# Performance work log

Hardware: AMD Instinct MI355X
Metric: run time of the kernel (lower is better)

The kernel has to match this reference:

```python
import jax, jax.numpy as jnp
import numpy as np

EPS = 1e-5
GROUPS = 4


def gconv1x1(x, w, b, groups):
    # x: [B,C,H,W]; w: [Cout, Cin//groups]; grouped 1x1 conv
    B, C, H, W = x.shape
    Co = w.shape[0]
    xg = x.reshape(B, groups, C // groups, H, W)
    wg = w.reshape(groups, Co // groups, C // groups)
    y = jnp.einsum('bgchw,goc->bgohw', xg, wg).reshape(B, Co, H, W)
    if b is not None:
        y = y + b[None, :, None, None]
    return y


def setup_inputs() -> dict:
    key = jax.random.key(0)
    ks = jax.random.split(key, 9)
    B, C, H, W = 8, 64, 160, 160
    Cq = C // 8
    s = 0.1
    return {
        'x': jax.random.normal(ks[0], (B, C, H, W), jnp.float32),
        'wq': jax.random.normal(ks[1], (Cq, C // GROUPS), jnp.float32) * s,
        'bq': jax.random.normal(ks[2], (Cq,), jnp.float32) * s,
        'wk': jax.random.normal(ks[3], (Cq, C // GROUPS), jnp.float32) * s,
        'bk': jax.random.normal(ks[4], (Cq,), jnp.float32) * s,
        'wv': jax.random.normal(ks[5], (C, C // GROUPS), jnp.float32) * s,
        'bv': jax.random.normal(ks[6], (C,), jnp.float32) * s,
        'gamma': jax.random.normal(ks[7], (1,), jnp.float32) * s,
        'w1d': jax.random.normal(ks[8], (C, C // GROUPS), jnp.float32) * s,
        'bn_w': jnp.ones((C,), jnp.float32),
        'bn_b': jnp.zeros((C,), jnp.float32),
    }


def reference(x, wq, bq, wk, bk, wv, bv, gamma, w1d, bn_w, bn_b):
    B, C, H, W = x.shape
    q = gconv1x1(x, wq, bq, GROUPS)   # [B,Cq,H,W]
    k = gconv1x1(x, wk, bk, GROUPS)   # [B,Cq,H,W]
    v = gconv1x1(x, wv, bv, GROUPS)   # [B,C,H,W]

    # column (H) attention energies with -inf diagonal (self excluded on H path)
    energy_H = jnp.einsum('bchw,bcjw->bhwj', q, k)  # [B,H,W,H]
    diag = jnp.where(jnp.eye(H, dtype=bool), -jnp.inf, 0.0).astype(x.dtype)
    energy_H = energy_H + diag[:, None, :]
    # row (W) attention energies
    energy_W = jnp.einsum('bchw,bchj->bhwj', q, k)  # [B,H,W,W]

    att = jax.nn.softmax(jnp.concatenate([energy_H, energy_W], axis=3), axis=3)
    att_H = att[..., :H]           # [B,H,W,H]
    att_W = att[..., H:]           # [B,H,W,W]

    out_H = jnp.einsum('bcjw,bhwj->bchw', v, att_H)
    out_W = jnp.einsum('bchj,bhwj->bchw', v, att_W)
    out = gamma[0] * (out_H + out_W)               # [B,C,H,W]

    # kernel-size-1 grouped conv1d (dilation irrelevant for k=1), no bias
    L = H * W
    o = out.reshape(B, GROUPS, C // GROUPS, L)
    w1g = w1d.reshape(GROUPS, C // GROUPS, C // GROUPS)
    o = jnp.einsum('bgcl,goc->bgol', o, w1g).reshape(B, C, L)

    # BatchNorm1d (training mode: batch stats over (B, L), biased variance)
    mean = jnp.mean(o, axis=(0, 2), keepdims=True)
    var = jnp.mean((o - mean) ** 2, axis=(0, 2), keepdims=True)
    o = (o - mean) / jnp.sqrt(var + EPS) * bn_w[None, :, None] + bn_b[None, :, None]

    o = o.reshape(B, C, H, W)
    return jax.nn.relu(o + x)
```

## Files before the change

### kernel.cpp

```cpp
#include <hip/hip_runtime.h>
#include <math.h>

#define B_ 8
#define C_ 64
#define H_ 160
#define W_ 160
#define HW_ (H_*W_)

typedef _Float16 h2 __attribute__((ext_vector_type(2)));
typedef _Float16 h8 __attribute__((ext_vector_type(8)));
typedef float f4v __attribute__((ext_vector_type(4)));
union H8u { h8 v; h2 h[4]; };

__device__ inline float fdot2(h2 a, h2 b, float c) {
    return __builtin_amdgcn_fdot2(a, b, c, false);
}
__device__ inline float dot16(const float4* xr, const float* wr, float acc) {
    float4 a = xr[0], b = xr[1], c = xr[2], d = xr[3];
    acc += a.x*wr[0]  + a.y*wr[1]  + a.z*wr[2]  + a.w*wr[3];
    acc += b.x*wr[4]  + b.y*wr[5]  + b.z*wr[6]  + b.w*wr[7];
    acc += c.x*wr[8]  + c.y*wr[9]  + c.z*wr[10] + c.w*wr[11];
    acc += d.x*wr[12] + d.y*wr[13] + d.z*wr[14] + d.w*wr[15];
    return acc;
}

static constexpr size_t N_PIX  = (size_t)B_*H_*W_;
static constexpr size_t N_FULL = (size_t)B_*H_*W_*C_;
static constexpr size_t OFF_OUTH  = 0;
static constexpr size_t OFF_VROW  = N_FULL/2;
static constexpr size_t OFF_QROW  = OFF_VROW + N_FULL/2;
static constexpr size_t OFF_KROW  = OFF_QROW + N_PIX*4;
static constexpr size_t OFF_MH    = OFF_KROW + N_PIX*4;
static constexpr size_t OFF_SH    = OFF_MH + N_PIX;
static constexpr size_t OFF_BNSUM = OFF_SH + N_PIX;
static constexpr size_t OFF_BNSQ  = OFF_BNSUM + 64;

__global__ __launch_bounds__(256,4) void qkv_kernel(
    const float* __restrict__ x,
    const float* __restrict__ wq, const float* __restrict__ bq,
    const float* __restrict__ wk, const float* __restrict__ bk,
    const float* __restrict__ wv, const float* __restrict__ bv,
    _Float16* __restrict__ qrow, _Float16* __restrict__ krow,
    _Float16* __restrict__ vrow)
{
    __shared__ __align__(16) float xs[128][68];
    const int tid = threadIdx.x;
    const int w0 = blockIdx.x * 32;
    const int h0 = blockIdx.y * 4;
    const int b  = blockIdx.z;

    const float* xb = x + (size_t)b*C_*HW_;
    for (int i = tid; i < 2048; i += 256) {
        int w4 = i & 7;
        int c  = ((i >> 3) & 7) | (((i >> 6) & 7) << 3);
        int hh = i >> 9;
        float4 v = *(const float4*)(xb + (size_t)c*HW_ + (size_t)(h0+hh)*W_ + w0 + w4*4);
        int pix = hh*32 + w4*4;
        xs[pix+0][c] = v.x; xs[pix+1][c] = v.y; xs[pix+2][c] = v.z; xs[pix+3][c] = v.w;
    }
    __syncthreads();

    float resv[32];
    {
        const int cp = tid & 31, pg = tid >> 5;
        const int c0 = 2*cp, g = c0 >> 4;
        float w0r[16], w1r[16];
        #pragma unroll
        for (int p = 0; p < 4; p++) {
            *(float4*)&w0r[4*p] = ((const float4*)(wv + c0*16))[p];
            *(float4*)&w1r[4*p] = ((const float4*)(wv + (c0+1)*16))[p];
        }
        const float b0 = bv[c0], b1 = bv[c0+1];
        #pragma unroll 4
        for (int i = 0; i < 16; i++) {
            int pix = pg*16 + i;
            const float4* xr = (const float4*)&xs[pix][g*16];
            resv[2*i]   = dot16(xr, w0r, b0);
            resv[2*i+1] = dot16(xr, w1r, b1);
        }
    }
    float resqk[8];
    {
        const int out = tid & 15, pg = tid >> 4;
        const int cq = out & 7, g = cq >> 1;
        const float* wp = ((out < 8) ? wq : wk) + cq*16;
        const float bb = (out < 8) ? bq[cq] : bk[cq];
        float wr[16];
        #pragma unroll
        for (int p = 0; p < 4; p++) *(float4*)&wr[4*p] = ((const float4*)wp)[p];
        #pragma unroll
        for (int i = 0; i < 8; i++) {
            int pix = pg*8 + i;
            resqk[i] = dot16((const float4*)&xs[pix][g*16], wr, bb);
        }
    }
    __syncthreads();

    unsigned* vs32 = (unsigned*)&xs[0][0];
    unsigned* qk32 = vs32 + 4096;
    {
        const int cp = tid & 31, pg = tid >> 5;
        #pragma unroll
        for (int i = 0; i < 16; i++) {
            int pix = pg*16 + i;
            h2 p; p.x = (_Float16)resv[2*i]; p.y = (_Float16)resv[2*i+1];
            vs32[pix*32 + cp] = *(unsigned*)&p;
        }
    }
    {
        const int out = tid & 15, pg = tid >> 4;
        _Float16* qks = (_Float16*)qk32;
        #pragma unroll
        for (int i = 0; i < 8; i++) qks[(pg*8+i)*16 + out] = (_Float16)resqk[i];
    }
    __syncthreads();

    unsigned* vrow32 = (unsigned*)vrow;
    for (int i = tid; i < 4096; i += 256) {
        int pix = i >> 5, cp = i & 31;
        size_t bp = ((size_t)b*H_ + h0 + (pix>>5))*W_ + w0 + (pix & 31);
        vrow32[bp*32 + cp] = vs32[i];
    }
    unsigned* qrow32 = (unsigned*)qrow;
    unsigned* krow32 = (unsigned*)krow;
    for (int i = tid; i < 1024; i += 256) {
        int pix = i >> 3, part = i & 7;
        size_t bp = ((size_t)b*H_ + h0 + (pix>>5))*W_ + w0 + (pix & 31);
        unsigned val = qk32[pix*8 + part];
        if (part < 4) qrow32[bp*4 + part]     = val;
        else          krow32[bp*4 + part - 4] = val;
    }
}

__global__ __launch_bounds__(256,4) void passA_kernel(
    const _Float16* __restrict__ qrow, const _Float16* __restrict__ krow,
    const _Float16* __restrict__ vrow,
    _Float16* __restrict__ outH, float* __restrict__ mH, float* __restrict__ sH)
{
    __shared__ __align__(16) _Float16 pool[10240];
    __shared__ __align__(16) _Float16 q2h[160][8];
    __shared__ __align__(16) _Float16 k2h[160][8];

    _Float16* v2s = pool;
    _Float16* Pts = pool;

    const int tid = threadIdx.x;
    const int b = blockIdx.x / W_;
    const int w = blockIdx.x % W_;

    if (tid < 160) {
        size_t bp = ((size_t)b*H_ + tid)*W_ + w;
        *(int4*)&q2h[tid][0] = *(const int4*)(qrow + bp*8);
        *(int4*)&k2h[tid][0] = *(const int4*)(krow + bp*8);
    }
    {
        const unsigned* vr32 = (const unsigned*)vrow;
        const int cp = tid & 31, hp0 = tid >> 5;
        #pragma unroll 2
        for (int it = 0; it < 10; it++) {
            int hp = hp0 + 8*it;
            int kt = hp >> 4, dqv = (hp >> 2) & 3, jj = 2*(hp & 3);
            size_t bp0 = ((size_t)b*H_ + 2*hp)*W_ + w;
            unsigned u0 = vr32[bp0*32 + cp];
            unsigned u1 = vr32[(bp0 + W_)*32 + cp];
            unsigned e  = __builtin_amdgcn_perm(u1, u0, 0x05040100);
            unsigned o  = __builtin_amdgcn_perm(u1, u0, 0x07060302);
            int base = ((kt*4 + dqv)*64 + 2*cp)*8 + jj;
            *(unsigned*)&v2s[base]     = e;
            *(unsigned*)&v2s[base + 8] = o;
        }
    }
    __syncthreads();

    const int u    = tid & 7;
    const int wl   = tid >> 3;
    const int lane = tid & 63;
    const int wid  = tid >> 6;
    const int cM   = wid*16 + (lane & 15);
    const int m_   = lane & 15;
    const int dq   = lane >> 4;

    h8 vfr[5];
    #pragma unroll
    for (int kt = 0; kt < 5; kt++)
        vfr[kt] = *(const h8*)&v2s[((kt*4 + dq)*64 + cM)*8];
    __syncthreads();

    for (int t = 0; t < 5; t++) {
        const int qh = t*32 + wl;
        H8u qr; qr.v = *(const h8*)&q2h[qh][0];
        float ev[20];
        float mloc = -1e30f;
        #pragma unroll 2
        for (int p = 0; p < 10; p++) {
            int j0 = 2*u + 16*p;
            H8u ka; ka.v = *(const h8*)&k2h[j0][0];
            H8u kb; kb.v = *(const h8*)&k2h[j0+1][0];
            float e0 = 0.f, e1 = 0.f;
            #pragma unroll
            for (int i = 0; i < 4; i++) {
                e0 = fdot2(qr.h[i], ka.h[i], e0);
                e1 = fdot2(qr.h[i], kb.h[i], e1);
            }
            ev[2*p] = e0; ev[2*p+1] = e1;
            if (j0   != qh) mloc = fmaxf(mloc, e0);
            if (j0+1 != qh) mloc = fmaxf(mloc, e1);
        }
        mloc = fmaxf(mloc, __shfl_xor(mloc, 1));
        mloc = fmaxf(mloc, __shfl_xor(mloc, 2));
        mloc = fmaxf(mloc, __shfl_xor(mloc, 4));
        float sloc = 0.f;
        #pragma unroll
        for (int p = 0; p < 10; p++) {
            int j0 = 2*u + 16*p;
            float p0 = (j0   == qh) ? 0.f : __expf(ev[2*p]   - mloc);
            float p1 = (j0+1 == qh) ? 0.f : __expf(ev[2*p+1] - mloc);
            sloc += p0 + p1;
            h2 pp; pp.x = (_Float16)p0; pp.y = (_Float16)p1;
            int idx = (((p>>1)*4 + (u>>2) + 2*(p&1))*32 + wl)*8 + 2*(u&3);
            *(unsigned*)&Pts[idx] = *(unsigned*)&pp;
        }
        sloc += __shfl_xor(sloc, 1);
        sloc += __shfl_xor(sloc, 2);
        sloc += __shfl_xor(sloc, 4);
        if (u == 0) {
            mH[((size_t)b*W_ + w)*H_ + qh] = mloc;
            sH[((size_t)b*W_ + w)*H_ + qh] = sloc;
        }
        __syncthreads();

        f4v acc0 = {0.f,0.f,0.f,0.f}, acc1 = {0.f,0.f,0.f,0.f};
        #pragma unroll
        for (int kt = 0; kt < 5; kt++) {
            h8 a0  = *(const h8*)&Pts[((kt*4 + dq)*32 + m_)*8];
            h8 a1  = *(const h8*)&Pts[((kt*4 + dq)*32 + 16 + m_)*8];
            acc0 = __builtin_amdgcn_mfma_f32_16x16x32_f16(a0, vfr[kt], acc0, 0, 0, 0);
            acc1 = __builtin_amdgcn_mfma_f32_16x16x32_f16(a1, vfr[kt], acc1, 0, 0, 0);
        }
        #pragma unroll
        for (int r = 0; r < 4; r++) {
            int r0 = t*32 + dq*4 + r;
            outH[(((size_t)b*H_ + r0     )*W_ + w)*64 + cM] = (_Float16)acc0[r];
            outH[(((size_t)b*H_ + r0 + 16)*W_ + w)*64 + cM] = (_Float16)acc1[r];
        }
        __syncthreads();
    }
}

__global__ __launch_bounds__(256,4) void passB_kernel(
    const _Float16* __restrict__ qrow, const _Float16* __restrict__ krow,
    const _Float16* vrow,
    const float* __restrict__ gamma, const float* __restrict__ w1d,
    const _Float16* __restrict__ outH, const float* __restrict__ mH, const float* __restrict__ sH,
    _Float16* o16, float* __restrict__ bnsum, float* __restrict__ bnsq)
{
    __shared__ __align__(16) _Float16 pool[10240];
    __shared__ __align__(16) _Float16 q2h[160][8];
    __shared__ __align__(16) _Float16 k2h[160][8];
    __shared__ float fHs[32], fWs[32];

    _Float16* v2s    = pool;
    _Float16* Pts    = pool;
    _Float16* stageh = pool + 5120;

    const int tid = threadIdx.x;
    const int b = blockIdx.x / H_;
    const int h = blockIdx.x % H_;
    const float gam = gamma[0];

    const int lane = tid & 63;
    const int wid  = tid >> 6;
    const int cM   = wid*16 + (lane & 15);
    const int m_   = lane & 15;
    const int dq   = lane >> 4;

    h2 w1h[8];
    #pragma unroll
    for (int p = 0; p < 8; p++) {
        float2 wpair = ((const float2*)(w1d + cM*16))[p];
        h2 wp; wp.x = (_Float16)wpair.x; wp.y = (_Float16)wpair.y;
        w1h[p] = wp;
    }

    const size_t rowbase = ((size_t)b*H_ + h)*W_;
    if (tid < 160) {
        size_t bp = rowbase + tid;
        *(int4*)&q2h[tid][0] = *(const int4*)(qrow + bp*8);
        *(int4*)&k2h[tid][0] = *(const int4*)(krow + bp*8);
    }
    {
        const unsigned* vr32 = (const unsigned*)vrow;
        const int cp = tid & 31, wp0 = tid >> 5;
        #pragma unroll 2
        for (int it = 0; it < 10; it++) {
            int wp = wp0 + 8*it;
            int kt = wp >> 4, dqv = (wp >> 2) & 3, jj = 2*(wp & 3);
            size_t bp0 = rowbase + 2*wp;
            unsigned u0 = vr32[bp0*32 + cp];
            unsigned u1 = vr32[(bp0 + 1)*32 + cp];
            unsigned e  = __builtin_amdgcn_perm(u1, u0, 0x05040100);
            unsigned o  = __builtin_amdgcn_perm(u1, u0, 0x07060302);
            int base = ((kt*4 + dqv)*64 + 2*cp)*8 + jj;
            *(unsigned*)&v2s[base]     = e;
            *(unsigned*)&v2s[base + 8] = o;
        }
    }
    __syncthreads();

    const int u  = tid & 7;
    const int wl = tid >> 3;

    h8 vfr[5];
    #pragma unroll
    for (int kt = 0; kt < 5; kt++)
        vfr[kt] = *(const h8*)&v2s[((kt*4 + dq)*64 + cM)*8];
    __syncthreads();

    float bnS = 0.f, bnS2 = 0.f;

    for (int t = 0; t < 5; t++) {
        const int qw = t*32 + wl;
        H8u qr; qr.v = *(const h8*)&q2h[qw][0];
        float ev[20];
        float mloc = -1e30f;
        #pragma unroll 2
        for (int p = 0; p < 10; p++) {
            int j0 = 2*u + 16*p;
            H8u ka; ka.v = *(const h8*)&k2h[j0][0];
            H8u kb; kb.v = *(const h8*)&k2h[j0+1][0];
            float e0 = 0.f, e1 = 0.f;
            #pragma unroll
            for (int i = 0; i < 4; i++) {
                e0 = fdot2(qr.h[i], ka.h[i], e0);
                e1 = fdot2(qr.h[i], kb.h[i], e1);
            }
            ev[2*p] = e0; ev[2*p+1] = e1;
            mloc = fmaxf(mloc, e0);
            mloc = fmaxf(mloc, e1);
        }
        mloc = fmaxf(mloc, __shfl_xor(mloc, 1));
        mloc = fmaxf(mloc, __shfl_xor(mloc, 2));
        mloc = fmaxf(mloc, __shfl_xor(mloc, 4));
        float sloc = 0.f;
        #pragma unroll
        for (int p = 0; p < 10; p++) {
            float p0 = __expf(ev[2*p]   - mloc);
            float p1 = __expf(ev[2*p+1] - mloc);
            sloc += p0 + p1;
            h2 pp; pp.x = (_Float16)p0; pp.y = (_Float16)p1;
            int idx = (((p>>1)*4 + (u>>2) + 2*(p&1))*32 + wl)*8 + 2*(u&3);
            *(unsigned*)&Pts[idx] = *(unsigned*)&pp;
        }
        sloc += __shfl_xor(sloc, 1);
        sloc += __shfl_xor(sloc, 2);
        sloc += __shfl_xor(sloc, 4);
        if (u == 0) {
            float mHv = mH[((size_t)b*W_ + qw)*H_ + h];
            float sHv = sH[((size_t)b*W_ + qw)*H_ + h];
            float M   = fmaxf(mHv, mloc);
            float eH  = __expf(mHv - M), eW = __expf(mloc - M);
            float inv = gam / (sHv*eH + sloc*eW);
            fHs[wl] = eH * inv;
            fWs[wl] = eW * inv;
        }
        float oh0[4], oh1[4];
        #pragma unroll
        for (int r = 0; r < 4; r++) {
            int rw0 = t*32 + dq*4 + r;
            oh0[r] = (float)outH[(rowbase + rw0     )*64 + cM];
            oh1[r] = (float)outH[(rowbase + rw0 + 16)*64 + cM];
        }
        __syncthreads();

        f4v acc0 = {0.f,0.f,0.f,0.f}, acc1 = {0.f,0.f,0.f,0.f};
        #pragma unroll
        for (int kt = 0; kt < 5; kt++) {
            h8 a0  = *(const h8*)&Pts[((kt*4 + dq)*32 + m_)*8];
            h8 a1  = *(const h8*)&Pts[((kt*4 + dq)*32 + 16 + m_)*8];
            acc0 = __builtin_amdgcn_mfma_f32_16x16x32_f16(a0, vfr[kt], acc0, 0, 0, 0);
            acc1 = __builtin_amdgcn_mfma_f32_16x16x32_f16(a1, vfr[kt], acc1, 0, 0, 0);
        }
        _Float16* st = &stageh[wid*576];
        #pragma unroll
        for (int r = 0; r < 4; r++) {
            int rl0 = dq*4 + r, rl1 = rl0 + 16;
            st[rl0*18 + m_] = (_Float16)(oh0[r]*fHs[rl0] + acc0[r]*fWs[rl0]);
            st[rl1*18 + m_] = (_Float16)(oh1[r]*fHs[rl1] + acc1[r]*fWs[rl1]);
        }
        #pragma unroll
        for (int r = 0; r < 4; r++) {
            #pragma unroll
            for (int mt = 0; mt < 2; mt++) {
                int rl = dq*4 + r + 16*mt;
                int rw = t*32 + rl;
                const h2* sp = (const h2*)&st[rl*18];
                float o = 0.f;
                #pragma unroll
                for (int p = 0; p < 8; p++) o = fdot2(sp[p], w1h[p], o);
                o16[(rowbase + rw)*64 + cM] = (_Float16)o;
                bnS  += o;
                bnS2 += o*o;
            }
        }
        __syncthreads();
    }
    bnS  += __shfl_xor(bnS, 16);  bnS  += __shfl_xor(bnS, 32);
    bnS2 += __shfl_xor(bnS2, 16); bnS2 += __shfl_xor(bnS2, 32);
    if (dq == 0) {
        atomicAdd(&bnsum[cM], bnS);
        atomicAdd(&bnsq[cM],  bnS2);
    }
}

__global__ __launch_bounds__(256) void final_kernel(
    const float* __restrict__ x, const _Float16* __restrict__ o16,
    const float* __restrict__ bnsum, const float* __restrict__ bnsq,
    const float* __restrict__ bn_w, const float* __restrict__ bn_b,
    float* __restrict__ out)
{
    __shared__ _Float16 olds[160*66];
    __shared__ float sc[64], sh[64];
    const int tid = threadIdx.x;
    const int b = blockIdx.x / H_, h = blockIdx.x % H_;
    if (tid < 64) {
        const float cnt = (float)(B_*H_*W_);
        float mean = bnsum[tid] / cnt;
        float var  = bnsq[tid] / cnt - mean*mean;
        float istd = rsqrtf(var + 1e-5f);
        float scl  = bn_w[tid] * istd;
        sc[tid] = scl;
        sh[tid] = bn_b[tid] - mean*scl;
    }
    const unsigned* op = (const unsigned*)(o16 + ((size_t)b*H_ + h)*W_*64);
    unsigned* ol32 = (unsigned*)olds;
    for (int i = tid; i < 5120; i += 256) {
        int w = i >> 5, c2 = i & 31;
        ol32[w*33 + c2] = op[i];
    }
    __syncthreads();
    const float* xr = x   + (size_t)b*C_*HW_ + (size_t)h*W_;
    float*       ob = out + (size_t)b*C_*HW_ + (size_t)h*W_;
    for (int i = tid; i < 64*160; i += 256) {
        int c = i / 160, w = i - c*160;
        float v = (float)olds[w*66 + c] * sc[c] + sh[c] + xr[(size_t)c*HW_ + w];
        ob[(size_t)c*HW_ + w] = fmaxf(v, 0.f);
    }
}

extern "C" void kernel_launch(void* const* d_in, const int* in_sizes, int n_in,
                              void* d_out, int out_size, void* d_ws, size_t ws_size,
                              hipStream_t stream)
{
    (void)in_sizes; (void)n_in; (void)out_size; (void)ws_size;
    const float* x     = (const float*)d_in[0];
    const float* wq    = (const float*)d_in[1];
    const float* bq    = (const float*)d_in[2];
    const float* wk    = (const float*)d_in[3];
    const float* bk    = (const float*)d_in[4];
    const float* wv    = (const float*)d_in[5];
    const float* bv    = (const float*)d_in[6];
    const float* gamma = (const float*)d_in[7];
    const float* w1d   = (const float*)d_in[8];
    const float* bn_w  = (const float*)d_in[9];
    const float* bn_b  = (const float*)d_in[10];

    float* ws = (float*)d_ws;
    _Float16* outH16 = (_Float16*)(ws + OFF_OUTH);
    _Float16* vrow   = (_Float16*)(ws + OFF_VROW);
    _Float16* qrow   = (_Float16*)(ws + OFF_QROW);
    _Float16* krow   = (_Float16*)(ws + OFF_KROW);
    float* mH    = ws + OFF_MH;
    float* sH    = ws + OFF_SH;
    float* bnsum = ws + OFF_BNSUM;
    float* bnsq  = ws + OFF_BNSQ;
    _Float16* o16 = vrow;

    hipMemsetAsync(bnsum, 0, 128*sizeof(float), stream);

    dim3 qgrid(W_/32, H_/4, B_);
    qkv_kernel<<<qgrid, 256, 0, stream>>>(x, wq, bq, wk, bk, wv, bv, qrow, krow, vrow);
    passA_kernel<<<B_*W_, 256, 0, stream>>>(qrow, krow, vrow, outH16, mH, sH);
    passB_kernel<<<B_*H_, 256, 0, stream>>>(qrow, krow, vrow, gamma, w1d,
                                            outH16, mH, sH, o16, bnsum, bnsq);
    final_kernel<<<B_*H_, 256, 0, stream>>>(x, o16, bnsum, bnsq, bn_w, bn_b, (float*)d_out);
}
```

Before: 246.7 us.

## Double-buffer softmax probabilities to overlap score computation with MFMA in attention passes

Both attention passes now double-buffer the probability tile in shared memory and software-pipeline the loop. Step t computes scores and softmax for tile t while the MFMA and output stage consume tile t-1. This removes one of the two barriers per iteration and lets VALU and matrix work interleave. In exchange it adds a dedicated stageh buffer and double-buffered fH/fW arrays in pass B, which raises LDS use and may lower occupancy.

```diff
diff --git a/kernel.cpp b/kernel.cpp
--- a/kernel.cpp
+++ b/kernel.cpp
@@ -142,7 +142,6 @@
     __shared__ __align__(16) _Float16 k2h[160][8];
 
     _Float16* v2s = pool;
-    _Float16* Pts = pool;
 
     const int tid = threadIdx.x;
     const int b = blockIdx.x / W_;
@@ -186,64 +185,68 @@
         vfr[kt] = *(const h8*)&v2s[((kt*4 + dq)*64 + cM)*8];
     __syncthreads();
 
-    for (int t = 0; t < 5; t++) {
-        const int qh = t*32 + wl;
-        H8u qr; qr.v = *(const h8*)&q2h[qh][0];
-        float ev[20];
-        float mloc = -1e30f;
-        #pragma unroll 2
-        for (int p = 0; p < 10; p++) {
-            int j0 = 2*u + 16*p;
-            H8u ka; ka.v = *(const h8*)&k2h[j0][0];
-            H8u kb; kb.v = *(const h8*)&k2h[j0+1][0];
-            float e0 = 0.f, e1 = 0.f;
-            #pragma unroll
-            for (int i = 0; i < 4; i++) {
-                e0 = fdot2(qr.h[i], ka.h[i], e0);
-                e1 = fdot2(qr.h[i], kb.h[i], e1);
-            }
-            ev[2*p] = e0; ev[2*p+1] = e1;
-            if (j0   != qh) mloc = fmaxf(mloc, e0);
-            if (j0+1 != qh) mloc = fmaxf(mloc, e1);
-        }
-        mloc = fmaxf(mloc, __shfl_xor(mloc, 1));
-        mloc = fmaxf(mloc, __shfl_xor(mloc, 2));
-        mloc = fmaxf(mloc, __shfl_xor(mloc, 4));
-        float sloc = 0.f;
-        #pragma unroll
-        for (int p = 0; p < 10; p++) {
-            int j0 = 2*u + 16*p;
-            float p0 = (j0   == qh) ? 0.f : __expf(ev[2*p]   - mloc);
-            float p1 = (j0+1 == qh) ? 0.f : __expf(ev[2*p+1] - mloc);
-            sloc += p0 + p1;
-            h2 pp; pp.x = (_Float16)p0; pp.y = (_Float16)p1;
-            int idx = (((p>>1)*4 + (u>>2) + 2*(p&1))*32 + wl)*8 + 2*(u&3);
-            *(unsigned*)&Pts[idx] = *(unsigned*)&pp;
-        }
-        sloc += __shfl_xor(sloc, 1);
-        sloc += __shfl_xor(sloc, 2);
-        sloc += __shfl_xor(sloc, 4);
-        if (u == 0) {
-            mH[((size_t)b*W_ + w)*H_ + qh] = mloc;
-            sH[((size_t)b*W_ + w)*H_ + qh] = sloc;
-        }
-        __syncthreads();
-
-        f4v acc0 = {0.f,0.f,0.f,0.f}, acc1 = {0.f,0.f,0.f,0.f};
-        #pragma unroll
-        for (int kt = 0; kt < 5; kt++) {
-            h8 a0  = *(const h8*)&Pts[((kt*4 + dq)*32 + m_)*8];
-            h8 a1  = *(const h8*)&Pts[((kt*4 + dq)*32 + 16 + m_)*8];
-            acc0 = __builtin_amdgcn_mfma_f32_16x16x32_f16(a0, vfr[kt], acc0, 0, 0, 0);
-            acc1 = __builtin_amdgcn_mfma_f32_16x16x32_f16(a1, vfr[kt], acc1, 0, 0, 0);
-        }
-        #pragma unroll
-        for (int r = 0; r < 4; r++) {
-            int r0 = t*32 + dq*4 + r;
-            outH[(((size_t)b*H_ + r0     )*W_ + w)*64 + cM] = (_Float16)acc0[r];
-            outH[(((size_t)b*H_ + r0 + 16)*W_ + w)*64 + cM] = (_Float16)acc1[r];
-        }
-        __syncthreads();
+    for (int t = 0; t <= 5; t++) {
+        if (t <= 4) {
+            _Float16* Pts = pool + (t & 1)*5120;
+            const int qh = t*32 + wl;
+            H8u qr; qr.v = *(const h8*)&q2h[qh][0];
+            float ev[20];
+            float mloc = -1e30f;
+            #pragma unroll 2
+            for (int p = 0; p < 10; p++) {
+                int j0 = 2*u + 16*p;
+                H8u ka; ka.v = *(const h8*)&k2h[j0][0];
+                H8u kb; kb.v = *(const h8*)&k2h[j0+1][0];
+                float e0 = 0.f, e1 = 0.f;
+                #pragma unroll
+                for (int i = 0; i < 4; i++) {
+                    e0 = fdot2(qr.h[i], ka.h[i], e0);
+                    e1 = fdot2(qr.h[i], kb.h[i], e1);
+                }
+                ev[2*p] = e0; ev[2*p+1] = e1;
+                if (j0   != qh) mloc = fmaxf(mloc, e0);
+                if (j0+1 != qh) mloc = fmaxf(mloc, e1);
+            }
+            mloc = fmaxf(mloc, __shfl_xor(mloc, 1));
+            mloc = fmaxf(mloc, __shfl_xor(mloc, 2));
+            mloc = fmaxf(mloc, __shfl_xor(mloc, 4));
+            float sloc = 0.f;
+            #pragma unroll
+            for (int p = 0; p < 10; p++) {
+                int j0 = 2*u + 16*p;
+                float p0 = (j0   == qh) ? 0.f : __expf(ev[2*p]   - mloc);
+                float p1 = (j0+1 == qh) ? 0.f : __expf(ev[2*p+1] - mloc);
+                sloc += p0 + p1;
+                h2 pp; pp.x = (_Float16)p0; pp.y = (_Float16)p1;
+                int idx = (((p>>1)*4 + (u>>2) + 2*(p&1))*32 + wl)*8 + 2*(u&3);
+                *(unsigned*)&Pts[idx] = *(unsigned*)&pp;
+            }
+            sloc += __shfl_xor(sloc, 1);
+            sloc += __shfl_xor(sloc, 2);
+            sloc += __shfl_xor(sloc, 4);
+            if (u == 0) {
+                mH[((size_t)b*W_ + w)*H_ + qh] = mloc;
+                sH[((size_t)b*W_ + w)*H_ + qh] = sloc;
+            }
+        }
+        if (t >= 1) {
+            const _Float16* Pts = pool + ((t-1) & 1)*5120;
+            f4v acc0 = {0.f,0.f,0.f,0.f}, acc1 = {0.f,0.f,0.f,0.f};
+            #pragma unroll
+            for (int kt = 0; kt < 5; kt++) {
+                h8 a0  = *(const h8*)&Pts[((kt*4 + dq)*32 + m_)*8];
+                h8 a1  = *(const h8*)&Pts[((kt*4 + dq)*32 + 16 + m_)*8];
+                acc0 = __builtin_amdgcn_mfma_f32_16x16x32_f16(a0, vfr[kt], acc0, 0, 0, 0);
+                acc1 = __builtin_amdgcn_mfma_f32_16x16x32_f16(a1, vfr[kt], acc1, 0, 0, 0);
+            }
+            #pragma unroll
+            for (int r = 0; r < 4; r++) {
+                int r0 = (t-1)*32 + dq*4 + r;
+                outH[(((size_t)b*H_ + r0     )*W_ + w)*64 + cM] = (_Float16)acc0[r];
+                outH[(((size_t)b*H_ + r0 + 16)*W_ + w)*64 + cM] = (_Float16)acc1[r];
+            }
+        }
+        if (t <= 4) __syncthreads();
     }
 }
 
@@ -255,13 +258,12 @@
     _Float16* o16, float* __restrict__ bnsum, float* __restrict__ bnsq)
 {
     __shared__ __align__(16) _Float16 pool[10240];
+    __shared__ __align__(16) _Float16 stageh[4*32*18];
     __shared__ __align__(16) _Float16 q2h[160][8];
     __shared__ __align__(16) _Float16 k2h[160][8];
-    __shared__ float fHs[32], fWs[32];
-
-    _Float16* v2s    = pool;
-    _Float16* Pts    = pool;
-    _Float16* stageh = pool + 5120;
+    __shared__ float fHs[2][32], fWs[2][32];
+
+    _Float16* v2s = pool;
 
     const int tid = threadIdx.x;
     const int b = blockIdx.x / H_;
@@ -318,91 +320,100 @@
 
     float bnS = 0.f, bnS2 = 0.f;
 
-    for (int t = 0; t < 5; t++) {
-        const int qw = t*32 + wl;
-        H8u qr; qr.v = *(const h8*)&q2h[qw][0];
-        float ev[20];
-        float mloc = -1e30f;
-        #pragma unroll 2
-        for (int p = 0; p < 10; p++) {
-            int j0 = 2*u + 16*p;
-            H8u ka; ka.v = *(const h8*)&k2h[j0][0];
-            H8u kb; kb.v = *(const h8*)&k2h[j0+1][0];
-            float e0 = 0.f, e1 = 0.f;
-            #pragma unroll
-            for (int i = 0; i < 4; i++) {
-                e0 = fdot2(qr.h[i], ka.h[i], e0);
-                e1 = fdot2(qr.h[i], kb.h[i], e1);
-            }
-            ev[2*p] = e0; ev[2*p+1] = e1;
-            mloc = fmaxf(mloc, e0);
-            mloc = fmaxf(mloc, e1);
-        }
-        mloc = fmaxf(mloc, __shfl_xor(mloc, 1));
-        mloc = fmaxf(mloc, __shfl_xor(mloc, 2));
-        mloc = fmaxf(mloc, __shfl_xor(mloc, 4));
-        float sloc = 0.f;
-        #pragma unroll
-        for (int p = 0; p < 10; p++) {
-            float p0 = __expf(ev[2*p]   - mloc);
-            float p1 = __expf(ev[2*p+1] - mloc);
-            sloc += p0 + p1;
-            h2 pp; pp.x = (_Float16)p0; pp.y = (_Float16)p1;
-            int idx = (((p>>1)*4 + (u>>2) + 2*(p&1))*32 + wl)*8 + 2*(u&3);
-            *(unsigned*)&Pts[idx] = *(unsigned*)&pp;
-        }
-        sloc += __shfl_xor(sloc, 1);
-        sloc += __shfl_xor(sloc, 2);
-        sloc += __shfl_xor(sloc, 4);
-        if (u == 0) {
-            float mHv = mH[((size_t)b*W_ + qw)*H_ + h];
-            float sHv = sH[((size_t)b*W_ + qw)*H_ + h];
-            float M   = fmaxf(mHv, mloc);
-            float eH  = __expf(mHv - M), eW = __expf(mloc - M);
-            float inv = gam / (sHv*eH + sloc*eW);
-            fHs[wl] = eH * inv;
-            fWs[wl] = eW * inv;
-        }
+    for (int t = 0; t <= 5; t++) {
         float oh0[4], oh1[4];
-        #pragma unroll
-        for (int r = 0; r < 4; r++) {
-            int rw0 = t*32 + dq*4 + r;
-            oh0[r] = (float)outH[(rowbase + rw0     )*64 + cM];
-            oh1[r] = (float)outH[(rowbase + rw0 + 16)*64 + cM];
-        }
-        __syncthreads();
-
-        f4v acc0 = {0.f,0.f,0.f,0.f}, acc1 = {0.f,0.f,0.f,0.f};
-        #pragma unroll
-        for (int kt = 0; kt < 5; kt++) {
-            h8 a0  = *(const h8*)&Pts[((kt*4 + dq)*32 + m_)*8];
-            h8 a1  = *(const h8*)&Pts[((kt*4 + dq)*32 + 16 + m_)*8];
-            acc0 = __builtin_amdgcn_mfma_f32_16x16x32_f16(a0, vfr[kt], acc0, 0, 0, 0);
-            acc1 = __builtin_amdgcn_mfma_f32_16x16x32_f16(a1, vfr[kt], acc1, 0, 0, 0);
-        }
-        _Float16* st = &stageh[wid*576];
-        #pragma unroll
-        for (int r = 0; r < 4; r++) {
-            int rl0 = dq*4 + r, rl1 = rl0 + 16;
-            st[rl0*18 + m_] = (_Float16)(oh0[r]*fHs[rl0] + acc0[r]*fWs[rl0]);
-            st[rl1*18 + m_] = (_Float16)(oh1[r]*fHs[rl1] + acc1[r]*fWs[rl1]);
-        }
-        #pragma unroll
-        for (int r = 0; r < 4; r++) {
-            #pragma unroll
-            for (int mt = 0; mt < 2; mt++) {
-                int rl = dq*4 + r + 16*mt;
-                int rw = t*32 + rl;
-                const h2* sp = (const h2*)&st[rl*18];
-                float o = 0.f;
+        if (t >= 1) {
+            #pragma unroll
+            for (int r = 0; r < 4; r++) {
+                int rw0 = (t-1)*32 + dq*4 + r;
+                oh0[r] = (float)outH[(rowbase + rw0     )*64 + cM];
+                oh1[r] = (float)outH[(rowbase + rw0 + 16)*64 + cM];
+            }
+        }
+        if (t <= 4) {
+            _Float16* Pts = pool + (t & 1)*5120;
+            const int qw = t*32 + wl;
+            H8u qr; qr.v = *(const h8*)&q2h[qw][0];
+            float ev[20];
+            float mloc = -1e30f;
+            #pragma unroll 2
+            for (int p = 0; p < 10; p++) {
+                int j0 = 2*u + 16*p;
+                H8u ka; ka.v = *(const h8*)&k2h[j0][0];
+                H8u kb; kb.v = *(const h8*)&k2h[j0+1][0];
+                float e0 = 0.f, e1 = 0.f;
                 #pragma unroll
-                for (int p = 0; p < 8; p++) o = fdot2(sp[p], w1h[p], o);
-                o16[(rowbase + rw)*64 + cM] = (_Float16)o;
-                bnS  += o;
-                bnS2 += o*o;
-            }
-        }
-        __syncthreads();
+                for (int i = 0; i < 4; i++) {
+                    e0 = fdot2(qr.h[i], ka.h[i], e0);
+                    e1 = fdot2(qr.h[i], kb.h[i], e1);
+                }
+                ev[2*p] = e0; ev[2*p+1] = e1;
+                mloc = fmaxf(mloc, e0);
+                mloc = fmaxf(mloc, e1);
+            }
+            mloc = fmaxf(mloc, __shfl_xor(mloc, 1));
+            mloc = fmaxf(mloc, __shfl_xor(mloc, 2));
+            mloc = fmaxf(mloc, __shfl_xor(mloc, 4));
+            float sloc = 0.f;
+            #pragma unroll
+            for (int p = 0; p < 10; p++) {
+                float p0 = __expf(ev[2*p]   - mloc);
+                float p1 = __expf(ev[2*p+1] - mloc);
+                sloc += p0 + p1;
+                h2 pp; pp.x = (_Float16)p0; pp.y = (_Float16)p1;
+                int idx = (((p>>1)*4 + (u>>2) + 2*(p&1))*32 + wl)*8 + 2*(u&3);
+                *(unsigned*)&Pts[idx] = *(unsigned*)&pp;
+            }
+            sloc += __shfl_xor(sloc, 1);
+            sloc += __shfl_xor(sloc, 2);
+            sloc += __shfl_xor(sloc, 4);
+            if (u == 0) {
+                float mHv = mH[((size_t)b*W_ + qw)*H_ + h];
+                float sHv = sH[((size_t)b*W_ + qw)*H_ + h];
+                float M   = fmaxf(mHv, mloc);
+                float eH  = __expf(mHv - M), eW = __expf(mloc - M);
+                float inv = gam / (sHv*eH + sloc*eW);
+                fHs[t & 1][wl] = eH * inv;
+                fWs[t & 1][wl] = eW * inv;
+            }
+        }
+        if (t >= 1) {
+            const int tp = t - 1;
+            const _Float16* Pts = pool + (tp & 1)*5120;
+            const float* fH = fHs[tp & 1];
+            const float* fW = fWs[tp & 1];
+            f4v acc0 = {0.f,0.f,0.f,0.f}, acc1 = {0.f,0.f,0.f,0.f};
+            #pragma unroll
+            for (int kt = 0; kt < 5; kt++) {
+                h8 a0  = *(const h8*)&Pts[((kt*4 + dq)*32 + m_)*8];
+                h8 a1  = *(const h8*)&Pts[((kt*4 + dq)*32 + 16 + m_)*8];
+                acc0 = __builtin_amdgcn_mfma_f32_16x16x32_f16(a0, vfr[kt], acc0, 0, 0, 0);
+                acc1 = __builtin_amdgcn_mfma_f32_16x16x32_f16(a1, vfr[kt], acc1, 0, 0, 0);
+            }
+            _Float16* st = &stageh[wid*576];
+            #pragma unroll
+            for (int r = 0; r < 4; r++) {
+                int rl0 = dq*4 + r, rl1 = rl0 + 16;
+                st[rl0*18 + m_] = (_Float16)(oh0[r]*fH[rl0] + acc0[r]*fW[rl0]);
+                st[rl1*18 + m_] = (_Float16)(oh1[r]*fH[rl1] + acc1[r]*fW[rl1]);
+            }
+            #pragma unroll
+            for (int r = 0; r < 4; r++) {
+                #pragma unroll
+                for (int mt = 0; mt < 2; mt++) {
+                    int rl = dq*4 + r + 16*mt;
+                    int rw = tp*32 + rl;
+                    const h2* sp = (const h2*)&st[rl*18];
+                    float o = 0.f;
+                    #pragma unroll
+                    for (int p = 0; p < 8; p++) o = fdot2(sp[p], w1h[p], o);
+                    o16[(rowbase + rw)*64 + cM] = (_Float16)o;
+                    bnS  += o;
+                    bnS2 += o*o;
+                }
+            }
+        }
+        if (t <= 4) __syncthreads();
     }
     bnS  += __shfl_xor(bnS, 16);  bnS  += __shfl_xor(bnS, 32);
     bnS2 += __shfl_xor(bnS2, 16); bnS2 += __shfl_xor(bnS2, 32);
@@ -475,7 +486,7 @@
     float* bnsq  = ws + OFF_BNSQ;
     _Float16* o16 = vrow;
 
-    hipMemsetAsync(bnsum, 0, 128*sizeof(float), stream);
+    (void)hipMemsetAsync(bnsum, 0, 128*sizeof(float), stream);
 
     dim3 qgrid(W_/32, H_/4, B_);
     qkv_kernel<<<qgrid, 256, 0, stream>>>(x, wq, bq, wk, bk, wv, bv, qrow, krow, vrow);
```

Measured after the change: 246.2 us. No clear change (-0.2%).
